# Kernel tuning notes

Measured on AMD Instinct MI355X. Metric: run time of the kernel, lower is better.

## Reference

```python
import jax, jax.numpy as jnp
import numpy as np

N, H, T, HID = 2, 8, 1024, 64
EMBED_DIM = H * HID  # 512, out_proj dim
EPS = 1e-6


def setup_inputs() -> dict:
    key = jax.random.key(0)
    kq, kk, kv, kw, kb = jax.random.split(key, 5)
    q = jax.random.normal(kq, (N, H, T, HID), jnp.float32)
    k = jax.random.normal(kk, (N, H, T, HID), jnp.float32)
    v = jax.random.normal(kv, (N, H, T, HID), jnp.float32)
    W_out = jax.random.normal(kw, (EMBED_DIM, EMBED_DIM), jnp.float32) / np.float32(np.sqrt(EMBED_DIM))
    b_out = jax.random.normal(kb, (EMBED_DIM,), jnp.float32) * 0.02
    return {"q": q, "k": k, "v": v, "W_out": W_out, "b_out": b_out}


def reference(q, k, v, W_out, b_out):
    # cosFormer attention, causal=True, act_fun='relu', has_outproj=True
    n, h, t, hid = q.shape
    nh = n * h
    m = t  # max(src_len, tgt_len)

    # q/k: permute(2,0,1,3).view(T,N,H*HID) -> relu -> view(-1,N*H,HID).transpose(0,1)
    # is equivalent to a direct reshape (N,H,T,HID)->(N*H,T,HID) since relu is elementwise.
    qr = jax.nn.relu(q).reshape(nh, t, hid)
    kr = jax.nn.relu(k).reshape(nh, t, hid)
    # v: original does v.view(-1, N*H, HID).transpose(0,1) WITHOUT permuting first
    # (reinterprets the (N,H,T,HID) buffer as (T, N*H, HID)); reproduce faithfully.
    vr = jnp.swapaxes(v.reshape(t, nh, hid), 0, 1)  # (NH, T, HID)

    # cos/sin position reweighting: weight_index = pi/2 * arange(1..m), used as /m
    idx = (np.float32(np.pi / 2) * jnp.arange(1, t + 1, dtype=q.dtype)) / m  # (T,)
    s = jnp.sin(idx)[None, :, None]
    c = jnp.cos(idx)[None, :, None]
    q_ = jnp.concatenate([qr * s, qr * c], axis=-1)  # (NH, T, 2*HID)
    k_ = jnp.concatenate([kr * s, kr * c], axis=-1)  # (NH, T, 2*HID)

    # causal path: cumulative outer products k_ (x) v, then contract with q_
    kv = jnp.einsum('nld,nlm->nldm', k_, vr)          # (NH, T, 2*HID, HID)
    kv_cum = jnp.cumsum(kv, axis=1)
    qkv = jnp.einsum('nld,nldm->nlm', q_, kv_cum)     # (NH, T, HID)
    k_cum = jnp.cumsum(k_, axis=1)
    denom = jnp.maximum(jnp.einsum('nld,nld->nl', q_, k_cum), EPS)
    attn = qkv / denom[..., None]                     # (NH, T, HID)

    # (NH,T,HID) -> (T,N,H*HID), out_proj, back to (N,H,T,HID)
    attn = jnp.swapaxes(attn, 0, 1).reshape(t, n, h * hid)
    attn = attn @ W_out.T + b_out
    context = attn.reshape(t, n, h, hid).transpose(1, 2, 0, 3)  # (N,H,T,HID)
    probs = jnp.zeros((n, h, t, t), q.dtype)
    return context, probs
```

## Files before the change

kernel.cpp:

```cpp
#include <hip/hip_runtime.h>

#define TSEQ 1024
#define HIDV 64
#define NHEADS 16
#define LCH 64
#define NCH 16
#define EMBED 512
#define CTX_FLOATS (NHEADS * TSEQ * HIDV)
#define EPSV 1e-6f
#define PIH 1.5707963267948966f

typedef short bf16x8 __attribute__((ext_vector_type(8)));
typedef float f32x4 __attribute__((ext_vector_type(4)));

__device__ __forceinline__ float relu_f(float x) { return fmaxf(x, 0.0f); }
__device__ __forceinline__ ushort f2bf(float f) {
    uint u = __float_as_uint(f);
    u += 0x7FFF + ((u >> 16) & 1);
    return (ushort)(u >> 16);
}
__device__ __forceinline__ float bf2f(ushort h) { return __uint_as_float(((uint)h) << 16); }
__device__ __forceinline__ uint pk2(float a, float b) {
    return (uint)f2bf(a) | ((uint)f2bf(b) << 16);
}

__global__ __launch_bounds__(256) void kA_chunksum(
    const float* __restrict__ K, const float* __restrict__ V,
    const float* __restrict__ W,
    ushort* __restrict__ S16, float* __restrict__ ksumws,
    ushort* __restrict__ W16, float4* __restrict__ probs4)
{
    __shared__ ushort kwT[128 * 88];
    __shared__ ushort vT1[32 * 88];
    const int bid = blockIdx.x;
    const int tid = threadIdx.x;

    {
        float4 z = make_float4(0.f, 0.f, 0.f, 0.f);
        size_t base = (size_t)bid * 2560 + tid;
        #pragma unroll
        for (int s = 0; s < 10; ++s) probs4[base + s * 256] = z;
    }
    {
        int g = bid * 128 + (tid & 127);
        if (tid < 128) {
            float4 w4 = *(const float4*)(W + (size_t)g * 4);
            *(uint2*)(W16 + (size_t)g * 4) = make_uint2(pk2(w4.x, w4.y), pk2(w4.z, w4.w));
        }
    }

    const int pair = bid >> 1, mh = bid & 1, m0b = mh * 32;
    const int b = pair >> 4, c = pair & 15;
    const int l0 = c * LCH;

    #pragma unroll
    for (int s = 0; s < 4; ++s) {
        int e = tid + s * 256;
        int i = e >> 4, d = (e & 15) * 4;
        float4 k4 = *(const float4*)(K + (size_t)(b * TSEQ + l0 + i) * HIDV + d);
        float si, ci;
        __sincosf(PIH * (float)(l0 + i + 1) * (1.0f / 1024.0f), &si, &ci);
        float kv[4] = {relu_f(k4.x), relu_f(k4.y), relu_f(k4.z), relu_f(k4.w)};
        #pragma unroll
        for (int j = 0; j < 4; ++j) {
            kwT[(d + j) * 88 + i] = f2bf(si * kv[j]);
            kwT[(d + 64 + j) * 88 + i] = f2bf(ci * kv[j]);
        }
    }
    #pragma unroll
    for (int s = 0; s < 2; ++s) {
        int e = tid + s * 256;
        int i = e >> 3, mf = (e & 7) * 4;
        float4 v4 = *(const float4*)(V + ((size_t)(l0 + i) * NHEADS + b) * HIDV + m0b + mf);
        vT1[(mf + 0) * 88 + i] = f2bf(v4.x);
        vT1[(mf + 1) * 88 + i] = f2bf(v4.y);
        vT1[(mf + 2) * 88 + i] = f2bf(v4.z);
        vT1[(mf + 3) * 88 + i] = f2bf(v4.w);
    }
    __syncthreads();

    const int w = tid >> 6, lane = tid & 63;
    const int quad = lane >> 4, l15 = lane & 15;

    bf16x8 bfv[2][2];
    #pragma unroll
    for (int mt = 0; mt < 2; ++mt)
        #pragma unroll
        for (int kk = 0; kk < 2; ++kk)
            bfv[mt][kk] = *(const bf16x8*)(vT1 + (mt * 16 + l15) * 88 + kk * 32 + quad * 8);

    f32x4 acc[2][2];
    #pragma unroll
    for (int ii = 0; ii < 2; ++ii)
        #pragma unroll
        for (int mt = 0; mt < 2; ++mt) acc[ii][mt] = (f32x4){0.f, 0.f, 0.f, 0.f};
    #pragma unroll
    for (int ii = 0; ii < 2; ++ii) {
        int itv = w + ii * 4;
        #pragma unroll
        for (int kk = 0; kk < 2; ++kk) {
            bf16x8 af = *(const bf16x8*)(kwT + (itv * 16 + l15) * 88 + kk * 32 + quad * 8);
            #pragma unroll
            for (int mt = 0; mt < 2; ++mt)
                acc[ii][mt] = __builtin_amdgcn_mfma_f32_16x16x32_bf16(af, bfv[mt][kk], acc[ii][mt], 0, 0, 0);
        }
    }
    ushort* SpT = S16 + (size_t)pair * 8192;
    #pragma unroll
    for (int ii = 0; ii < 2; ++ii)
        #pragma unroll
        for (int mt = 0; mt < 2; ++mt) {
            int m = m0b + mt * 16 + l15;
            int ddb = (w + ii * 4) * 16 + quad * 4;
            uint2 pk = make_uint2(pk2(acc[ii][mt][0], acc[ii][mt][1]),
                                  pk2(acc[ii][mt][2], acc[ii][mt][3]));
            *(uint2*)(SpT + m * 128 + ddb) = pk;
        }
    if (mh == 0 && tid < 128) {
        float ssum = 0.f;
        #pragma unroll
        for (int ss = 0; ss < 8; ++ss) {
            uint4 u = *(const uint4*)(kwT + tid * 88 + ss * 8);
            ssum += bf2f((ushort)(u.x & 0xffff)) + bf2f((ushort)(u.x >> 16));
            ssum += bf2f((ushort)(u.y & 0xffff)) + bf2f((ushort)(u.y >> 16));
            ssum += bf2f((ushort)(u.z & 0xffff)) + bf2f((ushort)(u.z >> 16));
            ssum += bf2f((ushort)(u.w & 0xffff)) + bf2f((ushort)(u.w >> 16));
        }
        ksumws[(size_t)pair * 128 + tid] = ssum;
    }
}

#define SMEM_BYTES 58368
#define OFF_QW 0
#define OFF_KW 17408
#define OFF_PT 34816
#define OFF_VT 43520
#define OFF_AM 48128
#define OFF_PSUM 57344
#define OFF_DENA 57856
#define OFF_DENI 58112

__global__ __launch_bounds__(256) void kB_attn(
    const float* __restrict__ Q, const float* __restrict__ K,
    const float* __restrict__ V,
    const ushort* __restrict__ S16, const float* __restrict__ ksumws,
    ushort* __restrict__ attn216, float4* __restrict__ probs4)
{
    __shared__ __align__(16) char smem[SMEM_BYTES];
    ushort* qw = (ushort*)(smem + OFF_QW);
    ushort* kw = (ushort*)(smem + OFF_KW);
    ushort* Pt = (ushort*)(smem + OFF_PT);
    ushort* vT = (ushort*)(smem + OFF_VT);
    ushort* Am = (ushort*)(smem + OFF_AM);
    float* psum = (float*)(smem + OFF_PSUM);
    float* denA = (float*)(smem + OFF_DENA);
    float* denI = (float*)(smem + OFF_DENI);

    const int bid = blockIdx.x;
    const int tid = threadIdx.x;
    const int w = tid >> 6, lane = tid & 63;
    const int quad = lane >> 4, l15 = lane & 15;

    {
        float4 z = make_float4(0.f, 0.f, 0.f, 0.f);
        size_t base = 1310720 + (size_t)bid * 2560 + tid;
        #pragma unroll
        for (int s = 0; s < 10; ++s) probs4[base + s * 256] = z;
    }

    const int pair = bid >> 1, mh = bid & 1, m0b = mh * 32;
    const int b = pair >> 4, c = pair & 15;
    const int l0 = c * LCH;

    {
        const int ml = tid >> 3, dd0 = (tid & 7) * 16;
        const ushort* Sb = S16 + ((size_t)b * NCH) * 8192 + (m0b + ml) * 128 + dd0;
        float accp[16];
        #pragma unroll
        for (int u = 0; u < 16; ++u) accp[u] = 0.f;
        for (int cp = 0; cp < c; ++cp) {
            const ushort* Sp = Sb + (size_t)cp * 8192;
            uint4 u0 = *(const uint4*)(Sp);
            uint4 u1 = *(const uint4*)(Sp + 8);
            uint uu[8] = {u0.x, u0.y, u0.z, u0.w, u1.x, u1.y, u1.z, u1.w};
            #pragma unroll
            for (int p = 0; p < 8; ++p) {
                accp[p * 2 + 0] += bf2f((ushort)(uu[p] & 0xffff));
                accp[p * 2 + 1] += bf2f((ushort)(uu[p] >> 16));
            }
        }
        uint pkv[8];
        #pragma unroll
        for (int p = 0; p < 8; ++p) pkv[p] = pk2(accp[p * 2], accp[p * 2 + 1]);
        *(uint4*)(Pt + ml * 136 + dd0) = make_uint4(pkv[0], pkv[1], pkv[2], pkv[3]);
        *(uint4*)(Pt + ml * 136 + dd0 + 8) = make_uint4(pkv[4], pkv[5], pkv[6], pkv[7]);
    }
    if (tid < 128) {
        float s = 0.f;
        const float* Kb = ksumws + (size_t)b * NCH * 128 + tid;
        for (int cp = 0; cp < c; ++cp) s += Kb[cp * 128];
        psum[tid] = s;
    }

    #pragma unroll
    for (int s = 0; s < 4; ++s) {
        int e = tid + s * 256;
        int i = e >> 4, d = (e & 15) * 4;
        float si, ci;
        __sincosf(PIH * (float)(l0 + i + 1) * (1.0f / 1024.0f), &si, &ci);
        float4 q4 = *(const float4*)(Q + (size_t)(b * TSEQ + l0 + i) * HIDV + d);
        float qv[4] = {relu_f(q4.x), relu_f(q4.y), relu_f(q4.z), relu_f(q4.w)};
        *(uint2*)(qw + i * 136 + d) = make_uint2(pk2(si * qv[0], si * qv[1]), pk2(si * qv[2], si * qv[3]));
        *(uint2*)(qw + i * 136 + 64 + d) = make_uint2(pk2(ci * qv[0], ci * qv[1]), pk2(ci * qv[2], ci * qv[3]));
        float4 k4 = *(const float4*)(K + (size_t)(b * TSEQ + l0 + i) * HIDV + d);
        float kv[4] = {relu_f(k4.x), relu_f(k4.y), relu_f(k4.z), relu_f(k4.w)};
        *(uint2*)(kw + i * 136 + d) = make_uint2(pk2(si * kv[0], si * kv[1]), pk2(si * kv[2], si * kv[3]));
        *(uint2*)(kw + i * 136 + 64 + d) = make_uint2(pk2(ci * kv[0], ci * kv[1]), pk2(ci * kv[2], ci * kv[3]));
    }
    #pragma unroll
    for (int s = 0; s < 2; ++s) {
        int e = tid + s * 256;
        int j = e >> 3, mf = (e & 7) * 4;
        float4 v4 = *(const float4*)(V + ((size_t)(l0 + j) * NHEADS + b) * HIDV + m0b + mf);
        vT[(mf + 0) * 72 + j] = f2bf(v4.x);
        vT[(mf + 1) * 72 + j] = f2bf(v4.y);
        vT[(mf + 2) * 72 + j] = f2bf(v4.z);
        vT[(mf + 3) * 72 + j] = f2bf(v4.w);
    }
    __syncthreads();

    const int it = w;
    bf16x8 af[4];
    #pragma unroll
    for (int kk = 0; kk < 4; ++kk)
        af[kk] = *(const bf16x8*)(qw + (it * 16 + l15) * 136 + kk * 32 + quad * 8);

    f32x4 accA[4];
    #pragma unroll
    for (int jt = 0; jt < 4; ++jt) {
        accA[jt] = (f32x4){0.f, 0.f, 0.f, 0.f};
        #pragma unroll
        for (int kk = 0; kk < 4; ++kk) {
            bf16x8 bf = *(const bf16x8*)(kw + (jt * 16 + l15) * 136 + kk * 32 + quad * 8);
            accA[jt] = __builtin_amdgcn_mfma_f32_16x16x32_bf16(af[kk], bf, accA[jt], 0, 0, 0);
        }
    }
    {
        float rsum[4] = {0.f, 0.f, 0.f, 0.f};
        #pragma unroll
        for (int jt = 0; jt < 4; ++jt) {
            int j = jt * 16 + l15;
            #pragma unroll
            for (int r = 0; r < 4; ++r) {
                int i = it * 16 + quad * 4 + r;
                float val = (j <= i) ? accA[jt][r] : 0.f;
                Am[i * 72 + j] = f2bf(val);
                rsum[r] += val;
            }
        }
        #pragma unroll
        for (int off = 1; off < 16; off <<= 1) {
            rsum[0] += __shfl_xor(rsum[0], off);
            rsum[1] += __shfl_xor(rsum[1], off);
            rsum[2] += __shfl_xor(rsum[2], off);
            rsum[3] += __shfl_xor(rsum[3], off);
        }
        if (l15 == 0) {
            #pragma unroll
            for (int r = 0; r < 4; ++r) denA[it * 16 + quad * 4 + r] = rsum[r];
        }
    }
    if (tid < 64) {
        float s = 0.f;
        #pragma unroll
        for (int ss = 0; ss < 16; ++ss) {
            uint4 u = *(const uint4*)(qw + tid * 136 + ss * 8);
            s += bf2f((ushort)(u.x & 0xffff)) * psum[ss * 8 + 0] + bf2f((ushort)(u.x >> 16)) * psum[ss * 8 + 1];
            s += bf2f((ushort)(u.y & 0xffff)) * psum[ss * 8 + 2] + bf2f((ushort)(u.y >> 16)) * psum[ss * 8 + 3];
            s += bf2f((ushort)(u.z & 0xffff)) * psum[ss * 8 + 4] + bf2f((ushort)(u.z >> 16)) * psum[ss * 8 + 5];
            s += bf2f((ushort)(u.w & 0xffff)) * psum[ss * 8 + 6] + bf2f((ushort)(u.w >> 16)) * psum[ss * 8 + 7];
        }
        denI[tid] = s;
    }
    __syncthreads();

    f32x4 accO[2];
    #pragma unroll
    for (int mm = 0; mm < 2; ++mm) {
        accO[mm] = (f32x4){0.f, 0.f, 0.f, 0.f};
        #pragma unroll
        for (int kk = 0; kk < 4; ++kk) {
            bf16x8 bp = *(const bf16x8*)(Pt + (mm * 16 + l15) * 136 + kk * 32 + quad * 8);
            accO[mm] = __builtin_amdgcn_mfma_f32_16x16x32_bf16(af[kk], bp, accO[mm], 0, 0, 0);
        }
    }
    bf16x8 aA[2];
    #pragma unroll
    for (int kk = 0; kk < 2; ++kk)
        aA[kk] = *(const bf16x8*)(Am + (it * 16 + l15) * 72 + kk * 32 + quad * 8);
    #pragma unroll
    for (int mm = 0; mm < 2; ++mm)
        #pragma unroll
        for (int kk = 0; kk < 2; ++kk) {
            bf16x8 bv = *(const bf16x8*)(vT + (mm * 16 + l15) * 72 + kk * 32 + quad * 8);
            accO[mm] = __builtin_amdgcn_mfma_f32_16x16x32_bf16(aA[kk], bv, accO[mm], 0, 0, 0);
        }

    const int nb = b >> 3, hh = b & 7;
    #pragma unroll
    for (int r = 0; r < 4; ++r) {
        int i = it * 16 + quad * 4 + r;
        float inv = 1.0f / fmaxf(denA[i] + denI[i], EPSV);
        #pragma unroll
        for (int mm = 0; mm < 2; ++mm) {
            int m = m0b + mm * 16 + l15;
            attn216[(size_t)((l0 + i) * 2 + nb) * EMBED + hh * 64 + m] = f2bf(accO[mm][r] * inv);
        }
    }
}

__global__ __launch_bounds__(256) void kC_outproj(
    const ushort* __restrict__ A16, const ushort* __restrict__ W16,
    const float* __restrict__ bias, float* __restrict__ out,
    float4* __restrict__ probs4)
{
    __shared__ ushort Ab[32 * 72];
    __shared__ ushort Bb[64 * 72];
    const int bid = blockIdx.x;
    const int tid = threadIdx.x;
    {
        float4 z = make_float4(0.f, 0.f, 0.f, 0.f);
        size_t base = 2621440 + (size_t)bid * 3072 + tid;
        #pragma unroll
        for (int s = 0; s < 12; ++s) probs4[base + s * 256] = z;
    }
    const int rt = bid >> 3, et = bid & 7;
    const int r0 = rt * 32, e0 = et * 64;
    const int w = tid >> 6, lane = tid & 63;
    const int quad = lane >> 4, l15 = lane & 15;
    const int it4 = w >> 1, jt0 = (w & 1) * 2;
    f32x4 acc4[2];
    acc4[0] = (f32x4){0.f, 0.f, 0.f, 0.f};
    acc4[1] = (f32x4){0.f, 0.f, 0.f, 0.f};

    for (int f0 = 0; f0 < EMBED; f0 += 64) {
        __syncthreads();
        {
            int rr = tid >> 3, ff = (tid & 7) * 8;
            *(uint4*)(Ab + rr * 72 + ff) = *(const uint4*)(A16 + (size_t)(r0 + rr) * EMBED + f0 + ff);
        }
        #pragma unroll
        for (int s = 0; s < 2; ++s) {
            int e = tid + s * 256;
            int rr = e >> 3, ff = (e & 7) * 8;
            *(uint4*)(Bb + rr * 72 + ff) = *(const uint4*)(W16 + (size_t)(e0 + rr) * EMBED + f0 + ff);
        }
        __syncthreads();
        bf16x8 af2[2];
        #pragma unroll
        for (int kk = 0; kk < 2; ++kk)
            af2[kk] = *(const bf16x8*)(Ab + (it4 * 16 + l15) * 72 + kk * 32 + quad * 8);
        #pragma unroll
        for (int jj = 0; jj < 2; ++jj) {
            int jt = jt0 + jj;
            #pragma unroll
            for (int kk = 0; kk < 2; ++kk) {
                bf16x8 bf = *(const bf16x8*)(Bb + (jt * 16 + l15) * 72 + kk * 32 + quad * 8);
                acc4[jj] = __builtin_amdgcn_mfma_f32_16x16x32_bf16(af2[kk], bf, acc4[jj], 0, 0, 0);
            }
        }
    }
    #pragma unroll
    for (int jj = 0; jj < 2; ++jj) {
        int e = e0 + (jt0 + jj) * 16 + l15;
        float be = bias[e];
        int h = e >> 6, m = e & 63;
        #pragma unroll
        for (int r = 0; r < 4; ++r) {
            int rr = r0 + it4 * 16 + quad * 4 + r;
            int t = rr >> 1, n = rr & 1;
            out[((size_t)(n * 8 + h) * TSEQ + t) * HIDV + m] = acc4[jj][r] + be;
        }
    }
}

extern "C" void kernel_launch(void* const* d_in, const int* in_sizes, int n_in,
                              void* d_out, int out_size, void* d_ws, size_t ws_size,
                              hipStream_t stream) {
    const float* q = (const float*)d_in[0];
    const float* k = (const float*)d_in[1];
    const float* v = (const float*)d_in[2];
    const float* W = (const float*)d_in[3];
    const float* bias = (const float*)d_in[4];
    float* out = (float*)d_out;
    float* ws = (float*)d_ws;

    ushort* S16 = (ushort*)ws;
    float* ksum_ws = ws + 1048576;
    ushort* attn216 = (ushort*)(ws + 1081344);
    ushort* W16 = (ushort*)(ws + 1605632);
    float4* probs4 = (float4*)(out + CTX_FLOATS);

    kA_chunksum<<<dim3(512), dim3(256), 0, stream>>>(k, v, W, S16, ksum_ws, W16, probs4);
    kB_attn<<<dim3(512), dim3(256), 0, stream>>>(q, k, v, S16, ksum_ws, attn216, probs4);
    kC_outproj<<<dim3(512), dim3(256), 0, stream>>>(attn216, W16, bias, out, probs4);
}
```

Before: 115.0 us.

## Use nontemporal stores, stage attention output in LDS, parallelize denominator, remap blocks

Turns the large zero-fill of probs and the output-projection results into nontemporal stores so the streaming writes bypass normal cache retention. In the attention kernel, each row's output tile is staged in shared memory so global writes become coalesced 16-byte stores instead of scattered 2-byte ones. The inter-chunk denominator is now computed by all waves from the MFMA A-fragments already held in registers, with a shuffle reduction, instead of by one wave doing serial LDS reads. Block indices at 256 and above are XOR-remapped, apparently to rebalance the uneven per-chunk prefix work. These add an extra barrier and reuse the qw shared-memory region, which must be dead by that point.

```diff
diff --git a/kernel.cpp b/kernel.cpp
--- a/kernel.cpp
+++ b/kernel.cpp
@@ -36,10 +36,11 @@
     const int tid = threadIdx.x;
 
     {
-        float4 z = make_float4(0.f, 0.f, 0.f, 0.f);
+        f32x4 z = {0.f, 0.f, 0.f, 0.f};
         size_t base = (size_t)bid * 2560 + tid;
         #pragma unroll
-        for (int s = 0; s < 10; ++s) probs4[base + s * 256] = z;
+        for (int s = 0; s < 10; ++s)
+            __builtin_nontemporal_store(z, (f32x4*)&probs4[base + s * 256]);
     }
     {
         int g = bid * 128 + (tid & 127);
@@ -156,16 +157,18 @@
     float* denA = (float*)(smem + OFF_DENA);
     float* denI = (float*)(smem + OFF_DENI);
 
-    const int bid = blockIdx.x;
+    const int rb = blockIdx.x;
+    const int bid = (rb < 256) ? rb : (rb ^ 30);
     const int tid = threadIdx.x;
     const int w = tid >> 6, lane = tid & 63;
     const int quad = lane >> 4, l15 = lane & 15;
 
     {
-        float4 z = make_float4(0.f, 0.f, 0.f, 0.f);
-        size_t base = 1310720 + (size_t)bid * 2560 + tid;
-        #pragma unroll
-        for (int s = 0; s < 10; ++s) probs4[base + s * 256] = z;
+        f32x4 z = {0.f, 0.f, 0.f, 0.f};
+        size_t base = 1310720 + (size_t)rb * 2560 + tid;
+        #pragma unroll
+        for (int s = 0; s < 10; ++s)
+            __builtin_nontemporal_store(z, (f32x4*)&probs4[base + s * 256]);
     }
 
     const int pair = bid >> 1, mh = bid & 1, m0b = mh * 32;
@@ -270,17 +273,20 @@
             for (int r = 0; r < 4; ++r) denA[it * 16 + quad * 4 + r] = rsum[r];
         }
     }
-    if (tid < 64) {
-        float s = 0.f;
-        #pragma unroll
-        for (int ss = 0; ss < 16; ++ss) {
-            uint4 u = *(const uint4*)(qw + tid * 136 + ss * 8);
-            s += bf2f((ushort)(u.x & 0xffff)) * psum[ss * 8 + 0] + bf2f((ushort)(u.x >> 16)) * psum[ss * 8 + 1];
-            s += bf2f((ushort)(u.y & 0xffff)) * psum[ss * 8 + 2] + bf2f((ushort)(u.y >> 16)) * psum[ss * 8 + 3];
-            s += bf2f((ushort)(u.z & 0xffff)) * psum[ss * 8 + 4] + bf2f((ushort)(u.z >> 16)) * psum[ss * 8 + 5];
-            s += bf2f((ushort)(u.w & 0xffff)) * psum[ss * 8 + 6] + bf2f((ushort)(u.w >> 16)) * psum[ss * 8 + 7];
-        }
-        denI[tid] = s;
+    {
+        float di = 0.f;
+        #pragma unroll
+        for (int kk = 0; kk < 4; ++kk) {
+            f32x4 p0 = *(const f32x4*)(psum + kk * 32 + quad * 8);
+            f32x4 p1 = *(const f32x4*)(psum + kk * 32 + quad * 8 + 4);
+            di += bf2f((ushort)af[kk][0]) * p0.x + bf2f((ushort)af[kk][1]) * p0.y;
+            di += bf2f((ushort)af[kk][2]) * p0.z + bf2f((ushort)af[kk][3]) * p0.w;
+            di += bf2f((ushort)af[kk][4]) * p1.x + bf2f((ushort)af[kk][5]) * p1.y;
+            di += bf2f((ushort)af[kk][6]) * p1.z + bf2f((ushort)af[kk][7]) * p1.w;
+        }
+        di += __shfl_xor(di, 16);
+        di += __shfl_xor(di, 32);
+        if (lane < 16) denI[it * 16 + l15] = di;
     }
     __syncthreads();
 
@@ -306,16 +312,21 @@
             accO[mm] = __builtin_amdgcn_mfma_f32_16x16x32_bf16(aA[kk], bv, accO[mm], 0, 0, 0);
         }
 
+    ushort* Orep = (ushort*)(smem + OFF_QW);
     const int nb = b >> 3, hh = b & 7;
     #pragma unroll
     for (int r = 0; r < 4; ++r) {
         int i = it * 16 + quad * 4 + r;
         float inv = 1.0f / fmaxf(denA[i] + denI[i], EPSV);
         #pragma unroll
-        for (int mm = 0; mm < 2; ++mm) {
-            int m = m0b + mm * 16 + l15;
-            attn216[(size_t)((l0 + i) * 2 + nb) * EMBED + hh * 64 + m] = f2bf(accO[mm][r] * inv);
-        }
+        for (int mm = 0; mm < 2; ++mm)
+            Orep[i * 40 + mm * 16 + l15] = f2bf(accO[mm][r] * inv);
+    }
+    __syncthreads();
+    {
+        int rr = tid >> 2, f = (tid & 3) * 8;
+        uint4 vv = *(const uint4*)(Orep + rr * 40 + f);
+        *(uint4*)(attn216 + (size_t)((l0 + rr) * 2 + nb) * EMBED + hh * 64 + m0b + f) = vv;
     }
 }
 
@@ -329,10 +340,11 @@
     const int bid = blockIdx.x;
     const int tid = threadIdx.x;
     {
-        float4 z = make_float4(0.f, 0.f, 0.f, 0.f);
+        f32x4 z = {0.f, 0.f, 0.f, 0.f};
         size_t base = 2621440 + (size_t)bid * 3072 + tid;
         #pragma unroll
-        for (int s = 0; s < 12; ++s) probs4[base + s * 256] = z;
+        for (int s = 0; s < 12; ++s)
+            __builtin_nontemporal_store(z, (f32x4*)&probs4[base + s * 256]);
     }
     const int rt = bid >> 3, et = bid & 7;
     const int r0 = rt * 32, e0 = et * 64;
@@ -379,7 +391,8 @@
         for (int r = 0; r < 4; ++r) {
             int rr = r0 + it4 * 16 + quad * 4 + r;
             int t = rr >> 1, n = rr & 1;
-            out[((size_t)(n * 8 + h) * TSEQ + t) * HIDV + m] = acc4[jj][r] + be;
+            __builtin_nontemporal_store(acc4[jj][r] + be,
+                &out[((size_t)(n * 8 + h) * TSEQ + t) * HIDV + m]);
         }
     }
 }
```

New measurement: 115.5 us. No clear change (+0.4%).
